# Optimization experiments

Hardware: AMD Instinct MI355X
Metric: run time of the kernel (lower is better)

The kernel has to match this reference:

```python
import jax, jax.numpy as jnp
import numpy as np

N, C, T, F = 32, 64, 256, 64  # batch, EEG channels, time samples, freq bands


def setup_inputs() -> dict:
    key = jax.random.key(0)
    X = jax.random.normal(key, (N, C, T, F), dtype=jnp.float32)
    gammad = jnp.zeros((), dtype=jnp.float32)  # learned scalar, init 'zeros'
    return {"X": X, "gammad": gammad}


def reference(X, gammad):
    # X: (N, C, T, F) -> (N, F, C, T)
    Xp = jnp.transpose(X, (0, 3, 1, 2))
    # squared norms per channel: (N, F, C, 1)
    R = jnp.sum(Xp * Xp, axis=-1, keepdims=True)
    # Gram matrix over time axis: (N, F, C, C)
    G = jnp.einsum('nfct,nfkt->nfck', Xp, Xp)
    # pairwise squared Euclidean distances between channels
    D = R - 2.0 * G + jnp.swapaxes(R, -1, -2)
    # strictly-upper-triangular entries (excludes diagonal), per (n, f)
    iu, ju = jnp.triu_indices(D.shape[-1], k=1)
    triu = jnp.sqrt(D[..., iu, ju])  # (N, F, C*(C-1)/2)
    # median bandwidth (tfp.stats.percentile q=50 uses 'nearest' interpolation)
    sigma = jnp.quantile(triu, 0.5, axis=-1, method='nearest')  # (N, F)
    denom = 2.0 * jnp.power(10.0, gammad) * jnp.square(sigma)   # (N, F)
    A = jnp.exp(-D / denom[..., None, None])  # (N, F, C, C) RBF affinity
    return A
```

## Files before the change

kernel.cpp:

```cpp
#include <hip/hip_runtime.h>
#include <stdint.h>

typedef _Float16 f16x8 __attribute__((ext_vector_type(8)));
typedef float f32x4 __attribute__((ext_vector_type(4)));

__device__ __forceinline__ f32x4 MF(f16x8 a, f16x8 b, f32x4 c) {
    return __builtin_amdgcn_mfma_f32_16x16x32_f16(a, b, c, 0, 0, 0);
}

__device__ __forceinline__ uint16_t h16(float v) {
    _Float16 h = (_Float16)v;
    return __builtin_bit_cast(uint16_t, h);
}

__device__ __forceinline__ uint16_t key16(float v) {
    _Float16 hx = (_Float16)fmaxf(v, 0.0f);
    return __builtin_bit_cast(uint16_t, hx);
}

__device__ __forceinline__ uint32_t pack2(float a, float b) {
    return (uint32_t)h16(a) | ((uint32_t)h16(b) << 16);
}

__global__ __launch_bounds__(256)
void gfc_prep(const float* __restrict__ X, uint16_t* __restrict__ W) {
    __shared__ uint16_t T[256 * 66];
    int n = blockIdx.x >> 6, c = blockIdx.x & 63;
    int tid = threadIdx.x;
    const float* src = X + ((size_t)n * 64 + c) * 16384;

    #pragma unroll
    for (int rb = 0; rb < 2; ++rb) {
        float4 v[8];
        #pragma unroll
        for (int i = 0; i < 8; ++i) {
            int o = (rb * 8 + i) * 256 + tid;
            v[i] = *(const float4*)(src + (size_t)o * 4);
        }
        #pragma unroll
        for (int i = 0; i < 8; ++i) {
            int o = (rb * 8 + i) * 256 + tid;
            int t = o >> 4, fj = o & 15;
            uint16_t* row = &T[t * 66 + fj * 4];
            row[0] = h16(v[i].x);
            row[1] = h16(v[i].y);
            row[2] = h16(v[i].z);
            row[3] = h16(v[i].w);
        }
    }
    __syncthreads();

    int f = tid >> 2, q = tid & 3;
    uint16_t* dst = W + (((size_t)n * 64 + f) * 64 + c) * 256 + q * 64;
    #pragma unroll
    for (int jj = 0; jj < 8; ++jj) {
        uint32_t w[4];
        #pragma unroll
        for (int p = 0; p < 4; ++p) {
            int t = q * 64 + jj * 8 + p * 2;
            uint32_t lo = T[t * 66 + f];
            uint32_t hi = T[(t + 1) * 66 + f];
            w[p] = lo | (hi << 16);
        }
        *(uint4*)(dst + jj * 8) = *(uint4*)w;
    }
}

__global__ __launch_bounds__(512, 2)
void gfc_main2(const uint16_t* __restrict__ W, const float* __restrict__ gp,
               float* __restrict__ out) {
    __shared__ float Rbuf[4][64];
    __shared__ uint32_t EX[8][1024];

    int j = blockIdx.x;
    int xcd = j & 7, r = j >> 3;
    int fq = r & 15, nh = r >> 4;
    int n = xcd * 4 + nh;
    int f0 = fq * 4;

    int tid = threadIdx.x;
    int wid = tid >> 6, lane = tid & 63;
    int w4 = wid & 3, hi = wid >> 2;
    int l4 = lane & 15, lg = lane >> 4;

    float p10 = exp2f(gp[0] * 3.3219280948873623f);
    const uint16_t* Wf = W + ((size_t)n * 64 + f0 + w4) * 16384;

    f32x4 dd[2][4];
    #pragma unroll
    for (int a = 0; a < 2; ++a)
        #pragma unroll
        for (int b = 0; b < 4; ++b) dd[a][b] = f32x4{0, 0, 0, 0};

    #pragma unroll
    for (int ks = 0; ks < 8; ++ks) {
        f16x8 fr[4];
        #pragma unroll
        for (int i2 = 0; i2 < 4; ++i2)
            fr[i2] = *(const f16x8*)(Wf + (i2 * 16 + l4) * 256 + ks * 32 + lg * 8);
        if (!hi) {
            #pragma unroll
            for (int tj = 0; tj < 4; ++tj) {
                dd[0][tj] = MF(fr[tj], fr[0], dd[0][tj]);
                dd[1][tj] = MF(fr[tj], fr[1], dd[1][tj]);
            }
        } else {
            #pragma unroll
            for (int tj = 0; tj < 4; ++tj) {
                dd[0][tj] = MF(fr[tj], fr[2], dd[0][tj]);
                dd[1][tj] = MF(fr[tj], fr[3], dd[1][tj]);
            }
        }
    }

    {
        f32x4 dg0 = hi ? dd[0][2] : dd[0][0];
        f32x4 dg1 = hi ? dd[1][3] : dd[1][1];
        if (lg == (l4 >> 2)) {
            int rr = l4 & 3;
            float v0 = rr == 0 ? dg0[0] : rr == 1 ? dg0[1] : rr == 2 ? dg0[2] : dg0[3];
            float v1 = rr == 0 ? dg1[0] : rr == 1 ? dg1[1] : rr == 2 ? dg1[2] : dg1[3];
            Rbuf[w4][(hi * 2) * 16 + l4] = v0;
            Rbuf[w4][(hi * 2 + 1) * 16 + l4] = v1;
        }
    }
    __syncthreads();

    float Rr0 = Rbuf[w4][(hi * 2) * 16 + l4];
    float Rr1 = Rbuf[w4][(hi * 2 + 1) * 16 + l4];
    #pragma unroll
    for (int tj = 0; tj < 4; ++tj) {
        f32x4 Rc = *(const f32x4*)&Rbuf[w4][tj * 16 + lg * 4];
        #pragma unroll
        for (int rr = 0; rr < 4; ++rr) {
            dd[0][tj][rr] = Rr0 + Rc[rr] - 2.0f * dd[0][tj][rr];
            dd[1][tj][rr] = Rr1 + Rc[rr] - 2.0f * dd[1][tj][rr];
        }
    }

    uint32_t pk[32];
    #pragma unroll
    for (int tt = 0; tt < 2; ++tt) {
        int row = (hi * 2 + tt) * 16 + l4;
        #pragma unroll
        for (int tj = 0; tj < 4; ++tj)
            #pragma unroll
            for (int rp = 0; rp < 2; ++rp) {
                int col0 = tj * 16 + lg * 4 + 2 * rp;
                uint32_t k0 = (row < col0)     ? key16(dd[tt][tj][2 * rp])     : 0x7FFFu;
                uint32_t k1 = (row < col0 + 1) ? key16(dd[tt][tj][2 * rp + 1]) : 0x7FFFu;
                pk[tt * 8 + tj * 2 + rp] = k0 | (k1 << 16);
            }
    }

    {
        uint32_t* mywr = EX[wid];
        #pragma unroll
        for (int e = 0; e < 16; ++e) mywr[e * 64 + lane] = pk[e];
        __syncthreads();
        const uint32_t* prd = EX[wid ^ 4];
        #pragma unroll
        for (int e = 0; e < 16; ++e) pk[16 + e] = prd[e * 64 + lane];
    }

    int u = 0;
    for (int bit = 14; bit >= 0; --bit) {
        uint32_t cand = (uint32_t)(u | (1 << bit));
        int cnt = 0;
        #pragma unroll
        for (int i = 0; i < 32; ++i) {
            cnt += ((pk[i] & 0xFFFFu) < cand) ? 1 : 0;
            cnt += ((pk[i] >> 16) < cand) ? 1 : 0;
        }
        #pragma unroll
        for (int off = 32; off; off >>= 1) cnt += __shfl_xor(cnt, off, 64);
        if (cnt <= 1008) u |= (1 << bit);
    }
    float sigma2 = (float)__builtin_bit_cast(_Float16, (uint16_t)u);
    float ninv = -1.0f / (2.0f * p10 * sigma2);

    float* op = out + ((size_t)(n * 64 + f0 + w4) << 12);
    #pragma unroll
    for (int tt = 0; tt < 2; ++tt) {
        int row = (hi * 2 + tt) * 16 + l4;
        #pragma unroll
        for (int tj = 0; tj < 4; ++tj) {
            float4 rv;
            rv.x = __expf(dd[tt][tj][0] * ninv);
            rv.y = __expf(dd[tt][tj][1] * ninv);
            rv.z = __expf(dd[tt][tj][2] * ninv);
            rv.w = __expf(dd[tt][tj][3] * ninv);
            *(float4*)(op + row * 64 + tj * 16 + lg * 4) = rv;
        }
    }
}

__global__ __launch_bounds__(512, 2)
void gfc_fb(const float* __restrict__ X, const float* __restrict__ gp,
            float* __restrict__ out) {
    __shared__ __align__(16) unsigned char XS[65536];
    __shared__ float Rbuf[4][64];
    int j = blockIdx.x;
    int xcd = j & 7, s = j >> 3;
    int gi = s >> 2, fq4 = s & 3;
    int g = gi * 8 + xcd;
    int n = g >> 2, f16g = g & 3;
    int f0 = f16g * 16 + fq4 * 4;
    int tid = threadIdx.x;
    int wid = tid >> 6, lane = tid & 63;
    int w4 = wid & 3, hi = wid >> 2;
    int l4 = lane & 15, lg = lane >> 4;
    float p10 = exp2f(gp[0] * 3.3219280948873623f);
    const float* Xn = X + (size_t)n * 1048576 + f0;
    f32x4 dd[2][4];
    #pragma unroll
    for (int a = 0; a < 2; ++a)
        #pragma unroll
        for (int b = 0; b < 4; ++b) dd[a][b] = f32x4{0, 0, 0, 0};
    float4 pv[8][2];
    auto load_chunk = [&](int t0) {
        #pragma unroll
        for (int k = 0; k < 8; ++k) {
            int c = k * 8 + wid;
            const float* p = Xn + (size_t)c * 16384 + t0 * 64 + lane * 128;
            pv[k][0] = *(const float4*)p;
            pv[k][1] = *(const float4*)(p + 64);
        }
    };
    auto write_chunk = [&]() {
        #pragma unroll
        for (int k = 0; k < 8; ++k) {
            int c = k * 8 + wid;
            int o = c * 256 + ((lane * 4) ^ ((c & 7) << 4));
            *(uint32_t*)(XS + o)         = pack2(pv[k][0].x, pv[k][1].x);
            *(uint32_t*)(XS + 16384 + o) = pack2(pv[k][0].y, pv[k][1].y);
            *(uint32_t*)(XS + 32768 + o) = pack2(pv[k][0].z, pv[k][1].z);
            *(uint32_t*)(XS + 49152 + o) = pack2(pv[k][0].w, pv[k][1].w);
        }
    };
    auto gram_buf = [&]() {
        const unsigned char* bp = XS + w4 * 16384;
        #pragma unroll
        for (int ks = 0; ks < 4; ++ks) {
            f16x8 fr[4];
            #pragma unroll
            for (int i2 = 0; i2 < 4; ++i2)
                fr[i2] = *(const f16x8*)(bp + (i2 * 16 + l4) * 256 +
                                         ((ks * 64 + lg * 16) ^ ((l4 & 7) << 4)));
            if (!hi) {
                #pragma unroll
                for (int tj = 0; tj < 4; ++tj) {
                    dd[0][tj] = MF(fr[tj], fr[0], dd[0][tj]);
                    dd[1][tj] = MF(fr[tj], fr[1], dd[1][tj]);
                }
            } else {
                #pragma unroll
                for (int tj = 0; tj < 4; ++tj) {
                    dd[0][tj] = MF(fr[tj], fr[2], dd[0][tj]);
                    dd[1][tj] = MF(fr[tj], fr[3], dd[1][tj]);
                }
            }
        }
    };
    load_chunk(0);
    write_chunk();
    load_chunk(128);
    __syncthreads();
    gram_buf();
    __syncthreads();
    write_chunk();
    __syncthreads();
    gram_buf();
    {
        f32x4 dg0 = hi ? dd[0][2] : dd[0][0];
        f32x4 dg1 = hi ? dd[1][3] : dd[1][1];
        if (lg == (l4 >> 2)) {
            int rr = l4 & 3;
            float v0 = rr == 0 ? dg0[0] : rr == 1 ? dg0[1] : rr == 2 ? dg0[2] : dg0[3];
            float v1 = rr == 0 ? dg1[0] : rr == 1 ? dg1[1] : rr == 2 ? dg1[2] : dg1[3];
            Rbuf[w4][(hi * 2) * 16 + l4] = v0;
            Rbuf[w4][(hi * 2 + 1) * 16 + l4] = v1;
        }
    }
    __syncthreads();
    float Rr0 = Rbuf[w4][(hi * 2) * 16 + l4];
    float Rr1 = Rbuf[w4][(hi * 2 + 1) * 16 + l4];
    #pragma unroll
    for (int tj = 0; tj < 4; ++tj) {
        f32x4 Rc = *(const f32x4*)&Rbuf[w4][tj * 16 + lg * 4];
        #pragma unroll
        for (int rr = 0; rr < 4; ++rr) {
            dd[0][tj][rr] = Rr0 + Rc[rr] - 2.0f * dd[0][tj][rr];
            dd[1][tj][rr] = Rr1 + Rc[rr] - 2.0f * dd[1][tj][rr];
        }
    }
    uint32_t pk[32];
    #pragma unroll
    for (int tt = 0; tt < 2; ++tt) {
        int row = (hi * 2 + tt) * 16 + l4;
        #pragma unroll
        for (int tj = 0; tj < 4; ++tj)
            #pragma unroll
            for (int rp = 0; rp < 2; ++rp) {
                int col0 = tj * 16 + lg * 4 + 2 * rp;
                uint32_t k0 = (row < col0)     ? key16(dd[tt][tj][2 * rp])     : 0x7FFFu;
                uint32_t k1 = (row < col0 + 1) ? key16(dd[tt][tj][2 * rp + 1]) : 0x7FFFu;
                pk[tt * 8 + tj * 2 + rp] = k0 | (k1 << 16);
            }
    }
    {
        uint32_t* base = (uint32_t*)(XS + w4 * 16384);
        uint32_t* mywr = base + hi * 1024;
        #pragma unroll
        for (int e = 0; e < 16; ++e) mywr[e * 64 + lane] = pk[e];
        __syncthreads();
        const uint32_t* prd = base + (hi ^ 1) * 1024;
        #pragma unroll
        for (int e = 0; e < 16; ++e) pk[16 + e] = prd[e * 64 + lane];
    }
    int u = 0;
    for (int bit = 14; bit >= 0; --bit) {
        uint32_t cand = (uint32_t)(u | (1 << bit));
        int cnt = 0;
        #pragma unroll
        for (int i = 0; i < 32; ++i) {
            cnt += ((pk[i] & 0xFFFFu) < cand) ? 1 : 0;
            cnt += ((pk[i] >> 16) < cand) ? 1 : 0;
        }
        #pragma unroll
        for (int off = 32; off; off >>= 1) cnt += __shfl_xor(cnt, off, 64);
        if (cnt <= 1008) u |= (1 << bit);
    }
    float sigma2 = (float)__builtin_bit_cast(_Float16, (uint16_t)u);
    float ninv = -1.0f / (2.0f * p10 * sigma2);
    float* op = out + ((size_t)(n * 64 + f0 + w4) << 12);
    #pragma unroll
    for (int tt = 0; tt < 2; ++tt) {
        int row = (hi * 2 + tt) * 16 + l4;
        #pragma unroll
        for (int tj = 0; tj < 4; ++tj) {
            float4 rv;
            rv.x = __expf(dd[tt][tj][0] * ninv);
            rv.y = __expf(dd[tt][tj][1] * ninv);
            rv.z = __expf(dd[tt][tj][2] * ninv);
            rv.w = __expf(dd[tt][tj][3] * ninv);
            *(float4*)(op + row * 64 + tj * 16 + lg * 4) = rv;
        }
    }
}

extern "C" void kernel_launch(void* const* d_in, const int* in_sizes, int n_in,
                              void* d_out, int out_size, void* d_ws, size_t ws_size,
                              hipStream_t stream) {
    (void)in_sizes; (void)n_in; (void)out_size;
    const float* X  = (const float*)d_in[0];
    const float* gp = (const float*)d_in[1];
    float* outp = (float*)d_out;
    if (ws_size >= (size_t)67108864) {
        uint16_t* W = (uint16_t*)d_ws;
        gfc_prep<<<2048, 256, 0, stream>>>(X, W);
        gfc_main2<<<512, 512, 0, stream>>>(W, gp, outp);
    } else {
        gfc_fb<<<512, 512, 0, stream>>>(X, gp, outp);
    }
}
```

Measured before the change: 76.56 us.

## Rewrite prep transpose with shuffles and pipeline fallback kernel via direct LDS loads

The prep kernel now builds fp16 pairs of adjacent time samples with a cross-lane shuffle. It stores them as packed 32-bit words in a swizzled LDS tile and writes the workspace with 16-byte stores. This is meant to cut LDS bank conflicts and the number of 16-bit shared-memory accesses in the transpose. Separately, the fallback kernel now streams X into a double-buffered LDS region, using global_load_lds where the builtin exists, and converts to fp16 when it reads fragments. That fallback only runs when the workspace is too small, and its extra barriers and per-element conversions may add overhead.

```diff
diff --git a/kernel.cpp b/kernel.cpp
--- a/kernel.cpp
+++ b/kernel.cpp
@@ -7,62 +7,75 @@
 __device__ __forceinline__ f32x4 MF(f16x8 a, f16x8 b, f32x4 c) {
     return __builtin_amdgcn_mfma_f32_16x16x32_f16(a, b, c, 0, 0, 0);
 }
-
 __device__ __forceinline__ uint16_t h16(float v) {
-    _Float16 h = (_Float16)v;
-    return __builtin_bit_cast(uint16_t, h);
-}
-
+    _Float16 h = (_Float16)v; return __builtin_bit_cast(uint16_t, h);
+}
 __device__ __forceinline__ uint16_t key16(float v) {
-    _Float16 hx = (_Float16)fmaxf(v, 0.0f);
-    return __builtin_bit_cast(uint16_t, hx);
-}
-
+    _Float16 h = (_Float16)fmaxf(v, 0.0f); return __builtin_bit_cast(uint16_t, h);
+}
 __device__ __forceinline__ uint32_t pack2(float a, float b) {
     return (uint32_t)h16(a) | ((uint32_t)h16(b) << 16);
 }
 
-__global__ __launch_bounds__(256)
-void gfc_prep(const float* __restrict__ X, uint16_t* __restrict__ W) {
-    __shared__ uint16_t T[256 * 66];
+#if defined(__has_builtin)
+# if __has_builtin(__builtin_amdgcn_global_load_lds)
+#  define HAVE_GLDS 1
+# endif
+#endif
+#ifndef HAVE_GLDS
+# define HAVE_GLDS 0
+#endif
+
+__global__ __launch_bounds__(256, 4)
+void gfc_prep(const float* __restrict__ X, uint32_t* __restrict__ W) {
+    __shared__ uint32_t Tp[128][64];
     int n = blockIdx.x >> 6, c = blockIdx.x & 63;
     int tid = threadIdx.x;
     const float* src = X + ((size_t)n * 64 + c) * 16384;
 
-    #pragma unroll
-    for (int rb = 0; rb < 2; ++rb) {
+    bool active = ((tid >> 4) & 1) == 0;
+    int f0 = 4 * (tid & 15);
+    #pragma unroll
+    for (int half = 0; half < 2; ++half) {
         float4 v[8];
         #pragma unroll
+        for (int i = 0; i < 8; ++i)
+            v[i] = *(const float4*)(src + (size_t)(half * 8 + i) * 1024 + tid * 4);
+        #pragma unroll
         for (int i = 0; i < 8; ++i) {
-            int o = (rb * 8 + i) * 256 + tid;
-            v[i] = *(const float4*)(src + (size_t)o * 4);
-        }
-        #pragma unroll
-        for (int i = 0; i < 8; ++i) {
-            int o = (rb * 8 + i) * 256 + tid;
-            int t = o >> 4, fj = o & 15;
-            uint16_t* row = &T[t * 66 + fj * 4];
-            row[0] = h16(v[i].x);
-            row[1] = h16(v[i].y);
-            row[2] = h16(v[i].z);
-            row[3] = h16(v[i].w);
+            float4 pv;
+            pv.x = __shfl_xor(v[i].x, 16, 64);
+            pv.y = __shfl_xor(v[i].y, 16, 64);
+            pv.z = __shfl_xor(v[i].z, 16, 64);
+            pv.w = __shfl_xor(v[i].w, 16, 64);
+            if (active) {
+                int p = 8 * (half * 8 + i) + (tid >> 5);
+                int col = f0 ^ (4 * ((p >> 2) & 7));
+                uint32_t w0 = pack2(v[i].x, pv.x);
+                uint32_t w1 = pack2(v[i].y, pv.y);
+                uint32_t w2 = pack2(v[i].z, pv.z);
+                uint32_t w3 = pack2(v[i].w, pv.w);
+                uint4 q; q.x = w0; q.y = w1; q.z = w2; q.w = w3;
+                *(uint4*)&Tp[p][col] = q;
+            }
         }
     }
     __syncthreads();
 
-    int f = tid >> 2, q = tid & 3;
-    uint16_t* dst = W + (((size_t)n * 64 + f) * 64 + c) * 256 + q * 64;
-    #pragma unroll
-    for (int jj = 0; jj < 8; ++jj) {
-        uint32_t w[4];
-        #pragma unroll
-        for (int p = 0; p < 4; ++p) {
-            int t = q * 64 + jj * 8 + p * 2;
-            uint32_t lo = T[t * 66 + f];
-            uint32_t hi = T[(t + 1) * 66 + f];
-            w[p] = lo | (hi << 16);
-        }
-        *(uint4*)(dst + jj * 8) = *(uint4*)w;
+    int wv = tid >> 6, l = tid & 63;
+    int k = l & 31, fh = l >> 5;
+    int sw = 4 * (k & 7);
+    #pragma unroll
+    for (int e = 0; e < 8; ++e) {
+        int f = wv * 16 + 2 * e + fh;
+        int col = f ^ sw;
+        uint4 q;
+        q.x = Tp[4 * k + 0][col];
+        q.y = Tp[4 * k + 1][col];
+        q.z = Tp[4 * k + 2][col];
+        q.w = Tp[4 * k + 3][col];
+        uint32_t* dst = W + ((size_t)(n * 64 + f) * 64 + c) * 128 + k * 4;
+        *(uint4*)dst = q;
     }
 }
 
@@ -210,67 +223,72 @@
     int wid = tid >> 6, lane = tid & 63;
     int w4 = wid & 3, hi = wid >> 2;
     int l4 = lane & 15, lg = lane >> 4;
+    int pos = lane & 31, cs = lane >> 5;
     float p10 = exp2f(gp[0] * 3.3219280948873623f);
-    const float* Xn = X + (size_t)n * 1048576 + f0;
+    const unsigned char* Xb = (const unsigned char*)(X + (size_t)n * 1048576 + f0);
     f32x4 dd[2][4];
     #pragma unroll
     for (int a = 0; a < 2; ++a)
         #pragma unroll
         for (int b = 0; b < 4; ++b) dd[a][b] = f32x4{0, 0, 0, 0};
-    float4 pv[8][2];
-    auto load_chunk = [&](int t0) {
-        #pragma unroll
-        for (int k = 0; k < 8; ++k) {
-            int c = k * 8 + wid;
-            const float* p = Xn + (size_t)c * 16384 + t0 * 64 + lane * 128;
-            pv[k][0] = *(const float4*)p;
-            pv[k][1] = *(const float4*)(p + 64);
+    auto stage = [&](int bsel, int T0) {
+        unsigned char* bb = XS + bsel * 32768;
+        #pragma unroll
+        for (int i = 0; i < 4; ++i) {
+            int c0 = wid * 8 + i * 2;
+            int c  = c0 + cs;
+            int tt = pos ^ (c & 15);
+            const unsigned char* gsrc = Xb + (size_t)c * 65536 + (size_t)(T0 + tt) * 256;
+#if HAVE_GLDS
+            __builtin_amdgcn_global_load_lds(
+                (const uint32_t __attribute__((address_space(1)))*)(uintptr_t)gsrc,
+                (uint32_t __attribute__((address_space(3)))*)(uintptr_t)(bb + c0 * 512),
+                16, 0, 0);
+#else
+            *(uint4*)(bb + c0 * 512 + lane * 16) = *(const uint4*)gsrc;
+#endif
         }
     };
-    auto write_chunk = [&]() {
-        #pragma unroll
-        for (int k = 0; k < 8; ++k) {
-            int c = k * 8 + wid;
-            int o = c * 256 + ((lane * 4) ^ ((c & 7) << 4));
-            *(uint32_t*)(XS + o)         = pack2(pv[k][0].x, pv[k][1].x);
-            *(uint32_t*)(XS + 16384 + o) = pack2(pv[k][0].y, pv[k][1].y);
-            *(uint32_t*)(XS + 32768 + o) = pack2(pv[k][0].z, pv[k][1].z);
-            *(uint32_t*)(XS + 49152 + o) = pack2(pv[k][0].w, pv[k][1].w);
+    auto gram = [&](int bsel) {
+        const float* B = (const float*)(XS + bsel * 32768);
+        f16x8 fr[4];
+        #pragma unroll
+        for (int i2 = 0; i2 < 4; ++i2) {
+            int c = i2 * 16 + l4;
+            int base = c * 128 + w4;
+            float v[8];
+            #pragma unroll
+            for (int jj = 0; jj < 8; ++jj) {
+                int tl = lg * 8 + jj;
+                v[jj] = B[base + (((tl ^ l4)) << 2)];
+            }
+            f16x8 f;
+            #pragma unroll
+            for (int jj = 0; jj < 8; ++jj) f[jj] = (_Float16)v[jj];
+            fr[i2] = f;
+        }
+        if (!hi) {
+            #pragma unroll
+            for (int tj = 0; tj < 4; ++tj) {
+                dd[0][tj] = MF(fr[tj], fr[0], dd[0][tj]);
+                dd[1][tj] = MF(fr[tj], fr[1], dd[1][tj]);
+            }
+        } else {
+            #pragma unroll
+            for (int tj = 0; tj < 4; ++tj) {
+                dd[0][tj] = MF(fr[tj], fr[2], dd[0][tj]);
+                dd[1][tj] = MF(fr[tj], fr[3], dd[1][tj]);
+            }
         }
     };
-    auto gram_buf = [&]() {
-        const unsigned char* bp = XS + w4 * 16384;
-        #pragma unroll
-        for (int ks = 0; ks < 4; ++ks) {
-            f16x8 fr[4];
-            #pragma unroll
-            for (int i2 = 0; i2 < 4; ++i2)
-                fr[i2] = *(const f16x8*)(bp + (i2 * 16 + l4) * 256 +
-                                         ((ks * 64 + lg * 16) ^ ((l4 & 7) << 4)));
-            if (!hi) {
-                #pragma unroll
-                for (int tj = 0; tj < 4; ++tj) {
-                    dd[0][tj] = MF(fr[tj], fr[0], dd[0][tj]);
-                    dd[1][tj] = MF(fr[tj], fr[1], dd[1][tj]);
-                }
-            } else {
-                #pragma unroll
-                for (int tj = 0; tj < 4; ++tj) {
-                    dd[0][tj] = MF(fr[tj], fr[2], dd[0][tj]);
-                    dd[1][tj] = MF(fr[tj], fr[3], dd[1][tj]);
-                }
-            }
-        }
-    };
-    load_chunk(0);
-    write_chunk();
-    load_chunk(128);
+    stage(0, 0);
     __syncthreads();
-    gram_buf();
-    __syncthreads();
-    write_chunk();
-    __syncthreads();
-    gram_buf();
+    #pragma unroll
+    for (int k = 0; k < 8; ++k) {
+        if (k < 7) stage((k + 1) & 1, (k + 1) * 32);
+        gram(k & 1);
+        if (k < 7) __syncthreads();
+    }
     {
         f32x4 dg0 = hi ? dd[0][2] : dd[0][0];
         f32x4 dg1 = hi ? dd[1][3] : dd[1][1];
@@ -309,7 +327,7 @@
             }
     }
     {
-        uint32_t* base = (uint32_t*)(XS + w4 * 16384);
+        uint32_t* base = (uint32_t*)(XS + w4 * 8192);
         uint32_t* mywr = base + hi * 1024;
         #pragma unroll
         for (int e = 0; e < 16; ++e) mywr[e * 64 + lane] = pk[e];
@@ -357,9 +375,8 @@
     const float* gp = (const float*)d_in[1];
     float* outp = (float*)d_out;
     if (ws_size >= (size_t)67108864) {
-        uint16_t* W = (uint16_t*)d_ws;
-        gfc_prep<<<2048, 256, 0, stream>>>(X, W);
-        gfc_main2<<<512, 512, 0, stream>>>(W, gp, outp);
+        gfc_prep<<<2048, 256, 0, stream>>>(X, (uint32_t*)d_ws);
+        gfc_main2<<<512, 512, 0, stream>>>((const uint16_t*)d_ws, gp, outp);
     } else {
         gfc_fb<<<512, 512, 0, stream>>>(X, gp, outp);
     }
```

New measurement: 72.30 us. 5.6% less time.
